# Kernel tuning notes

Measured on AMD Instinct MI355X. Metric: run time of the kernel, lower is better.

The kernel has to match this reference:

```python
import jax, jax.numpy as jnp
import numpy as np

jax.config.update("jax_enable_x64", True)  # int64 needed for packed lattice keys

BILATERAL = True
THETA_ALPHA = 80.0
THETA_BETA = 13.0
THETA_GAMMA = 3.0


def setup_inputs() -> dict:
    key = jax.random.key(0)
    k1, k2 = jax.random.split(key)
    x = jax.random.normal(k1, (2, 21, 256, 256), dtype=jnp.float32)
    image = jax.random.uniform(k2, (2, 3, 256, 256), dtype=jnp.float32) * 255.0  # RGB guide in [0,255)
    return {"x": x, "image": image}


def _permutohedral_filter(vals, feats, bid):
    """Permutohedral lattice Gaussian filtering (Adams et al. / DenseCRF).
    vals: (N, C) float32 signal, feats: (N, d) float32 features, bid: (N,) int64 batch id.
    """
    N, C = vals.shape
    d = feats.shape[1]
    dp1 = d + 1
    # --- elevate features onto the hyperplane sum=0 in R^{d+1} ---
    inv_std = np.sqrt(2.0 / 3.0) * dp1
    scale = (inv_std / np.sqrt((np.arange(d) + 1.0) * (np.arange(d) + 2.0))).astype(np.float32)
    E = np.zeros((dp1, d), np.float32)  # elevation matrix matching DenseCRF recursion
    E[0, :] = 1.0
    for j in range(1, dp1):
        E[j, j:] = 1.0
        E[j, j - 1] = -float(j)
    elevated = (feats * scale) @ E.T  # (N, d+1)

    # --- closest zero-colored lattice point (rem0) and rank ---
    v = elevated / dp1
    up = jnp.ceil(v) * dp1
    down = jnp.floor(v) * dp1
    rem0 = jnp.where(up - elevated < elevated - down, up, down)  # (N, d+1)
    ssum = jnp.round(jnp.sum(rem0, axis=1) / dp1).astype(jnp.int32)  # (N,)

    di = elevated - rem0
    m = jnp.arange(dp1)
    upper = m[None, :] > m[:, None]
    lt = di[:, :, None] < di[:, None, :]
    le = di[:, :, None] <= di[:, None, :]
    contrib = jnp.where(upper[None], lt, le) & (m[None, :] != m[:, None])[None]
    rank = jnp.sum(contrib, axis=2).astype(jnp.int32) + ssum[:, None]  # (N, d+1)
    rem0 = jnp.where(rank < 0, rem0 + dp1, jnp.where(rank > d, rem0 - dp1, rem0))
    rank = jnp.where(rank < 0, rank + dp1, jnp.where(rank > d, rank - dp1, rank))

    # --- barycentric weights (N, d+1) ---
    t = (elevated - rem0) / dp1
    oh = (jax.nn.one_hot(d - rank, d + 2, dtype=vals.dtype)
          - jax.nn.one_hot(d + 1 - rank, d + 2, dtype=vals.dtype))
    bary = jnp.einsum('ni,nij->nj', t, oh)  # (N, d+2)
    bary = jnp.concatenate([bary[:, :1] + 1.0 + bary[:, d + 1:d + 2], bary[:, 1:dp1]], axis=1)

    # --- simplex vertex keys via canonical simplex ---
    rem0i = jnp.round(rem0).astype(jnp.int64)
    r = jnp.arange(dp1, dtype=jnp.int64)
    keys = (rem0i[:, None, :] + r[None, :, None]
            - dp1 * (rank[:, None, :].astype(jnp.int64) > (d - r)[None, :, None]))  # (N, d+1, d+1)

    OFF = jnp.int64(2048)
    BASE = jnp.int64(4096)
    pw = BASE ** jnp.arange(d, dtype=jnp.int64)
    BSHIFT = jnp.int64(4096 ** d)  # batch-id slot above coordinate bits

    def pack(k, b):  # pack first d coords (sum-zero => last is redundant) + batch id
        return jnp.sum((k[..., :d] + OFF) * pw, axis=-1) + b * BSHIFT

    packed = pack(keys, bid[:, None]).reshape(-1)  # (N*(d+1),)
    M = int(packed.shape[0])
    FILL = jnp.iinfo(jnp.int64).max
    uk = jnp.unique(packed, size=M, fill_value=FILL)  # sorted unique lattice keys (hash table)
    idx = jnp.searchsorted(uk, packed)  # (N*(d+1),) index of each vertex

    # --- splat ---
    lat = jnp.zeros((M, C), vals.dtype).at[idx].add(
        (bary[:, :, None] * vals[:, None, :]).reshape(-1, C))

    # decode unique keys back to full (d+1)-dim coords + batch id
    ub = uk // BSHIFT
    remk = uk % BSHIFT
    coords = ((remk[:, None] // pw[None, :]) % BASE) - OFF  # (M, d)
    coords = jnp.concatenate([coords, -jnp.sum(coords, axis=1, keepdims=True)], axis=1)  # (M, d+1)

    def lookup(q, lat_cur):
        pos = jnp.clip(jnp.searchsorted(uk, q), 0, M - 1)
        ok = uk[pos] == q
        return jnp.where(ok[:, None], lat_cur[pos], 0.0)

    # --- blur: [1 2 1]/2 along each of the d+1 lattice directions ---
    for j in range(dp1):
        off = np.ones((dp1,), np.int64)
        off[j] = -d
        off = jnp.asarray(off)
        n1 = pack(coords + off[None, :], ub)
        n2 = pack(coords - off[None, :], ub)
        lat = lat + 0.5 * (lookup(n1, lat) + lookup(n2, lat))

    # --- slice ---
    alpha = 1.0 / (1.0 + 2.0 ** (-d))
    sliced = lat[idx].reshape(N, dp1, C)
    return alpha * jnp.einsum('nr,nrc->nc', bary, sliced)


def _forward(x, image):
    B, C, H, W = x.shape
    x_nhwc = jnp.transpose(x, (0, 2, 3, 1)).reshape(-1, C)
    im_nhwc = jnp.transpose(image, (0, 2, 3, 1))
    ys, xs = jnp.meshgrid(jnp.arange(H, dtype=x.dtype), jnp.arange(W, dtype=x.dtype), indexing='ij')
    if BILATERAL:
        pos = jnp.broadcast_to(jnp.stack([xs, ys], axis=-1) / THETA_ALPHA, (B, H, W, 2))
        feats = jnp.concatenate([pos, im_nhwc / THETA_BETA], axis=-1)  # d = 5
    else:
        feats = jnp.broadcast_to(jnp.stack([xs, ys], axis=-1) / THETA_GAMMA, (B, H, W, 2))  # d = 2
    d = feats.shape[-1]
    bid = jnp.repeat(jnp.arange(B, dtype=jnp.int64), H * W)  # keep per-image lattices separate
    out = _permutohedral_filter(x_nhwc, feats.reshape(B * H * W, d), bid)
    return jnp.transpose(out.reshape(B, H, W, C), (0, 3, 1, 2))


def reference(x, image):
    return _forward(x, image)
```

## Files before the change

kernel.cpp:

```cpp
#include <hip/hip_runtime.h>
#include <hip/hip_fp16.h>
#include <stdint.h>

#define BB   2
#define CC   21
#define HCP  32
#define NPT  (BB*256*256)
#define DP1  6
#define NV   (NPT*DP1)
#define TS   (1u<<20)
#define TMASK (TS-1)
#define EMPTYK 0xFFFFFFFFFFFFFFFFULL
#define NBLK (NV/1024)
#define NBUCK 32768
#define KEYMASK ((1ULL<<41)-1ULL)


__device__ __forceinline__ uint64_t hmix(uint64_t x){
  x ^= x >> 33; x *= 0xff51afd7ed558ccdULL;
  x ^= x >> 33; x *= 0xc4ceb9fe1a85ec53ULL;
  x ^= x >> 33; return x;
}

__device__ __forceinline__ int hlookup(const unsigned long long* __restrict__ hs,
                                       uint64_t key){
  uint32_t h = (uint32_t)hmix(key) & TMASK;
  for (;;){
    unsigned long long e = hs[h];
    if (e == EMPTYK) return -1;
    if ((e & KEYMASK) == (unsigned long long)key) return (int)(e >> 41);
    h = (h + 1) & TMASK;
  }
}

__device__ __forceinline__ void row_load(const __half* p, float2 f[12]){
  const uint4* p4 = (const uint4*)p;
  #pragma unroll
  for (int i=0;i<3;i++){
    uint4 r = p4[i];
    const __half2* h = (const __half2*)&r;
    #pragma unroll
    for (int j=0;j<4;j++) f[i*4+j] = __half22float2(h[j]);
  }
}
__device__ __forceinline__ void row_store(__half* p, const float2 f[12]){
  uint4* p4 = (uint4*)p;
  #pragma unroll
  for (int i=0;i<3;i++){
    uint4 r;
    __half2* h = (__half2*)&r;
    #pragma unroll
    for (int j=0;j<4;j++) h[j] = __floats2half2_rn(f[i*4+j].x, f[i*4+j].y);
    p4[i] = r;
  }
}

__global__ __launch_bounds__(256) void k_tx(const float* __restrict__ xin,
      __half* __restrict__ xt){
  int n = blockIdx.x*256 + threadIdx.x;
  if (n >= NPT) return;
  int b = n >> 16, pix = n & 65535;
  const float* xb = xin + (((size_t)b*CC) << 16) + pix;
  float2 v[12];
  #pragma unroll
  for (int q=0;q<12;q++){
    int c0 = 2*q, c1 = 2*q+1;
    v[q].x = (c0 < CC) ? xb[(size_t)c0 << 16] : 0.f;
    v[q].y = (c1 < CC) ? xb[(size_t)c1 << 16] : 0.f;
  }
  row_store(xt + (size_t)n*HCP, v);
}

__global__ __launch_bounds__(256) void k_build(const float* __restrict__ img,
      unsigned long long* __restrict__ hs,
      int* __restrict__ hist,
      unsigned long long* __restrict__ pkeys,
      float* __restrict__ pbary,
      int* __restrict__ hslot){
  int n = blockIdx.x*256 + threadIdx.x;
  if (n >= NPT) return;
  int b = n >> 16, pix = n & 65535;
  int y = pix >> 8, x = pix & 255;
  const float sc0 = 3.4641016151377544f, sc1 = 2.0f, sc2 = 1.4142135623730951f,
              sc3 = 1.0954451150103321f, sc4 = 0.8944271909999159f;
  size_t ib = ((size_t)b*3) << 16;
  float f0 = ((float)x / 80.0f) * sc0;
  float f1 = ((float)y / 80.0f) * sc1;
  float f2 = (img[ib + pix]          / 13.0f) * sc2;
  float f3 = (img[ib + 65536 + pix]  / 13.0f) * sc3;
  float f4 = (img[ib + 131072 + pix] / 13.0f) * sc4;
  float E[6];
  {
    float s4 = f4;
    E[5] = -5.0f*f4;
    E[4] = -4.0f*f3 + s4;
    float s3 = f3 + s4;
    E[3] = -3.0f*f2 + s3;
    float s2 = f2 + s3;
    E[2] = -2.0f*f1 + s2;
    float s1 = f1 + s2;
    E[1] = -f0 + s1;
    E[0] =  f0 + s1;
  }
  float rem0[6], di[6]; int rk[6];
  float ssf = 0.f;
  #pragma unroll
  for (int i=0;i<6;i++){
    float v  = E[i] / 6.0f;
    float up = ceilf(v)*6.0f, dn = floorf(v)*6.0f;
    float r0 = (up - E[i] < E[i] - dn) ? up : dn;
    rem0[i] = r0; di[i] = E[i] - r0; ssf += r0;
  }
  int ssum = (int)rintf(ssf / 6.0f);
  #pragma unroll
  for (int i=0;i<6;i++){
    int c = ssum;
    #pragma unroll
    for (int k=0;k<6;k++){
      if (k==i) continue;
      bool t = (k>i) ? (di[i] < di[k]) : (di[i] <= di[k]);
      c += t ? 1 : 0;
    }
    rk[i] = c;
  }
  #pragma unroll
  for (int i=0;i<6;i++){
    if      (rk[i] < 0){ rk[i] += 6; rem0[i] += 6.0f; }
    else if (rk[i] > 5){ rk[i] -= 6; rem0[i] -= 6.0f; }
  }
  float bar[7] = {0,0,0,0,0,0,0};
  #pragma unroll
  for (int i=0;i<6;i++){
    float t = (E[i] - rem0[i]) / 6.0f;
    #pragma unroll
    for (int j=0;j<7;j++){
      bar[j] += ((5-rk[i])==j) ? t : 0.0f;
      bar[j] -= ((6-rk[i])==j) ? t : 0.0f;
    }
  }
  float w0 = bar[0] + 1.0f + bar[6];
  int ri[5];
  #pragma unroll
  for (int i=0;i<5;i++) ri[i] = (int)rintf(rem0[i]);
  uint64_t bbit = ((uint64_t)b) << 40;
  #pragma unroll
  for (int r=0;r<6;r++){
    uint64_t key = bbit;
    #pragma unroll
    for (int i=0;i<5;i++){
      int k = ri[i] + r - ((rk[i] > 5-r) ? 6 : 0);
      key |= ((uint64_t)(uint32_t)(k + 128) & 0xFFULL) << (8*i);
    }
    pkeys[n*6+r] = key;
    pbary[n*6+r] = (r==0) ? w0 : bar[r];
    uint64_t ins = key | ((uint64_t)(uint32_t)n << 41);
    uint32_t h = (uint32_t)hmix(key) & TMASK;
    for (;;){
      unsigned long long seen = hs[h];
      if (seen != EMPTYK && (seen & KEYMASK) == (unsigned long long)key) break;
      if (seen == EMPTYK){
        unsigned long long prev = atomicCAS(&hs[h], EMPTYK, (unsigned long long)ins);
        if (prev == EMPTYK){
          atomicAdd(&hist[n >> 2], 1);
          break;
        }
        if ((prev & KEYMASK) == (unsigned long long)key) break;
      }
      h = (h + 1) & TMASK;
    }
    hslot[n*6+r] = (int)h;
  }
}

__global__ __launch_bounds__(1024) void k_scan_small(const int* __restrict__ hist,
      int* __restrict__ boff, int* __restrict__ bcur, int* __restrict__ counter){
  __shared__ int s[1024];
  int t = threadIdx.x;
  int base = t * (NBUCK/1024);
  int loc[NBUCK/1024];
  int sum = 0;
  #pragma unroll
  for (int i=0;i<NBUCK/1024;i++){ loc[i] = hist[base+i]; sum += loc[i]; }
  s[t] = sum;
  __syncthreads();
  #pragma unroll
  for (int o=1;o<1024;o<<=1){
    int add = (t>=o) ? s[t-o] : 0;
    __syncthreads();
    s[t] += add;
    __syncthreads();
  }
  int run = s[t] - sum;
  #pragma unroll
  for (int i=0;i<NBUCK/1024;i++){ boff[base+i] = run; bcur[base+i] = run; run += loc[i]; }
  if (t == 1023) counter[0] = run;
}

__global__ __launch_bounds__(1024) void k_place(unsigned long long* __restrict__ hs,
      int* __restrict__ bcur,
      unsigned long long* __restrict__ latkeys){
  uint32_t s = blockIdx.x*1024 + threadIdx.x;
  unsigned long long e = hs[s];
  if (e == EMPTYK) return;
  int nown = (int)(e >> 41);
  int idx = atomicAdd(&bcur[nown >> 2], 1);
  unsigned long long key = e & KEYMASK;
  hs[s] = key | ((unsigned long long)idx << 41);
  latkeys[idx] = key;
}

__global__ __launch_bounds__(256) void k_nbr(const unsigned long long* __restrict__ hs,
      const unsigned long long* __restrict__ latkeys, const int* __restrict__ counter,
      uint2* __restrict__ nbr){
  int m = blockIdx.x*256 + threadIdx.x;
  if (m >= *counter) return;
  uint64_t key = (uint64_t)latkeys[m];
  const unsigned long long S5 = (1ULL<<32)+(1ULL<<24)+(1ULL<<16)+(1ULL<<8)+1ULL;
  #pragma unroll
  for (int j=0;j<6;j++){
    unsigned long long delta = (j<5) ? (S5 - (6ULL << (8*j))) : S5;
    int i1 = hlookup(hs, key + delta);
    int i2 = hlookup(hs, key - delta);
    nbr[(size_t)j*NV + m] = make_uint2((uint32_t)(i1+1), (uint32_t)(i2+1));
  }
}

__global__ __launch_bounds__(256) void k_find(const unsigned long long* __restrict__ hs,
      const int* __restrict__ hslot,
      int* __restrict__ pidx, int* __restrict__ cnt){
  int t = blockIdx.x*256 + threadIdx.x;
  if (t >= NV) return;
  int i = (int)(hs[hslot[t]] >> 41);
  pidx[t] = i;
  atomicAdd(&cnt[i], 1);
}

__global__ __launch_bounds__(1024) void k_scan1(const int* __restrict__ cnt,
      int* __restrict__ off, int* __restrict__ bsum){
  __shared__ int s[1024];
  int t = threadIdx.x;
  int i = blockIdx.x*1024 + t;
  int v = cnt[i];
  s[t] = v;
  __syncthreads();
  #pragma unroll
  for (int o=1;o<1024;o<<=1){
    int add = (t>=o) ? s[t-o] : 0;
    __syncthreads();
    s[t] += add;
    __syncthreads();
  }
  off[i] = s[t] - v;
  if (t==1023) bsum[blockIdx.x] = s[t];
}

__global__ __launch_bounds__(1024) void k_scan2(int* __restrict__ bsum){
  __shared__ int s[1024];
  int t = threadIdx.x;
  int v = (t < NBLK) ? bsum[t] : 0;
  s[t] = v;
  __syncthreads();
  #pragma unroll
  for (int o=1;o<1024;o<<=1){
    int add = (t>=o) ? s[t-o] : 0;
    __syncthreads();
    s[t] += add;
    __syncthreads();
  }
  if (t < NBLK) bsum[t] = s[t] - v;
}

__global__ __launch_bounds__(1024) void k_scan3(int* __restrict__ off,
      const int* __restrict__ bsum, int* __restrict__ cur){
  int i = blockIdx.x*1024 + threadIdx.x;
  int o = off[i] + bsum[blockIdx.x];
  off[i] = o;
  cur[i] = o;
}

__global__ __launch_bounds__(256) void k_scatter(const int* __restrict__ pidx,
      const float* __restrict__ pbary, int* __restrict__ cur, uint2* __restrict__ plist2){
  int t = blockIdx.x*256 + threadIdx.x;
  if (t >= NV) return;
  int idx = pidx[t];
  int pos = atomicAdd(&cur[idx], 1);
  plist2[pos] = make_uint2((uint32_t)(t/6), __float_as_uint(pbary[t]));
}

__global__ __launch_bounds__(256) void k_splat2(const __half* __restrict__ xt,
      const int* __restrict__ off, const int* __restrict__ cnt,
      const uint2* __restrict__ plist2, const int* __restrict__ counter,
      __half* __restrict__ lat){
  int m = blockIdx.x*256 + threadIdx.x;
  if (m >= *counter) return;
  float2 acc[12];
  #pragma unroll
  for (int q=0;q<12;q++) acc[q] = make_float2(0.f,0.f);
  int c0 = off[m], k = cnt[m];
  for (int e=c0; e<c0+k; ++e){
    uint2 pv = plist2[e];
    float w = __uint_as_float(pv.y);
    float2 xr[12];
    row_load(xt + (size_t)pv.x*HCP, xr);
    #pragma unroll
    for (int q=0;q<12;q++){
      acc[q].x = fmaf(w, xr[q].x, acc[q].x);
      acc[q].y = fmaf(w, xr[q].y, acc[q].y);
    }
  }
  row_store(lat + (size_t)m*HCP, acc);
}

__global__ __launch_bounds__(256) void k_blur(const uint2* __restrict__ nbrj,
      const int* __restrict__ counter, const __half* __restrict__ src,
      __half* __restrict__ dst){
  int m = blockIdx.x*256 + threadIdx.x;
  if (m >= *counter) return;
  uint2 e = nbrj[m];
  float2 a[12], u[12], v[12];
  #pragma unroll
  for (int q=0;q<12;q++){ u[q] = make_float2(0.f,0.f); v[q] = make_float2(0.f,0.f); }
  row_load(src + (size_t)m*HCP, a);
  if (e.x) row_load(src + (size_t)(e.x-1u)*HCP, u);
  if (e.y) row_load(src + (size_t)(e.y-1u)*HCP, v);
  float2 r[12];
  #pragma unroll
  for (int q=0;q<12;q++){
    r[q].x = a[q].x + 0.5f*(u[q].x + v[q].x);
    r[q].y = a[q].y + 0.5f*(u[q].y + v[q].y);
  }
  row_store(dst + (size_t)m*HCP, r);
}

__global__ __launch_bounds__(256) void k_slice(const __half* __restrict__ lat,
      const int* __restrict__ pidx, const float* __restrict__ pbary,
      float* __restrict__ out){
  int n = blockIdx.x*256 + threadIdx.x;
  if (n >= NPT) return;
  float2 acc[12];
  #pragma unroll
  for (int q=0;q<12;q++) acc[q] = make_float2(0.f,0.f);
  #pragma unroll
  for (int r=0;r<6;r++){
    int idx = pidx[n*6+r]; float w = pbary[n*6+r];
    float2 L[12];
    row_load(lat + (size_t)idx*HCP, L);
    #pragma unroll
    for (int q=0;q<12;q++){
      acc[q].x = fmaf(w, L[q].x, acc[q].x);
      acc[q].y = fmaf(w, L[q].y, acc[q].y);
    }
  }
  int b = n >> 16, pix = n & 65535;
  float* ob = out + (((size_t)b*CC) << 16) + pix;
  const float alpha = 0.9696969696969697f;
  #pragma unroll
  for (int c=0;c<CC;c++){
    float val = (c & 1) ? acc[c>>1].y : acc[c>>1].x;
    ob[(size_t)c << 16] = alpha * val;
  }
}

extern "C" void kernel_launch(void* const* d_in, const int* in_sizes, int n_in,
                              void* d_out, int out_size, void* d_ws, size_t ws_size,
                              hipStream_t stream){
  const float* xin = (const float*)d_in[0];
  const float* img = (const float*)d_in[1];
  float* out = (float*)d_out;

  char* p = (char*)d_ws;
  auto carve = [&](size_t bytes)->char*{
    char* r = p; p += (bytes + 255) & ~(size_t)255; return r;
  };
  unsigned long long* hs      = (unsigned long long*)carve((size_t)TS*8);
  unsigned long long* latkeys = (unsigned long long*)carve((size_t)NV*8);
  int*                counter = (int*)               carve(256);
  unsigned long long* pkeys   = (unsigned long long*)carve((size_t)NV*8);
  int*                pidx    = (int*)               carve((size_t)NV*4);
  float*              pbary   = (float*)             carve((size_t)NV*4);
  int*                hslot   = (int*)               carve((size_t)NV*4);
  int*                cnt     = (int*)               carve((size_t)NV*4);
  int*                off     = (int*)               carve((size_t)NV*4);
  int*                cur     = (int*)               carve((size_t)NV*4);
  int*                bsum    = (int*)               carve((size_t)NBLK*4);
  int*                hist    = (int*)               carve((size_t)NBUCK*4);
  int*                boff    = (int*)               carve((size_t)NBUCK*4);
  int*                bcur    = (int*)               carve((size_t)NBUCK*4);
  uint2*              nbr     = (uint2*)             carve((size_t)6*NV*8);
  __half*             latA    = (__half*)            carve((size_t)NV*HCP*2);
  __half*             latB    = (__half*)            carve((size_t)NV*HCP*2);

  __half* xt     = latB;
  uint2* plist2  = (uint2*)pkeys;

  hipMemsetAsync(hs, 0xFF, (size_t)TS*8, stream);
  hipMemsetAsync(cnt, 0, (size_t)NV*4, stream);
  hipMemsetAsync(hist, 0, (size_t)NBUCK*4, stream);

  k_tx        <<<NPT/256, 256, 0, stream>>>(xin, xt);
  k_build     <<<NPT/256, 256, 0, stream>>>(img, hs, hist, pkeys, pbary, hslot);
  k_scan_small<<<1,      1024, 0, stream>>>(hist, boff, bcur, counter);
  k_place     <<<TS/1024,1024, 0, stream>>>(hs, bcur, latkeys);
  k_nbr       <<<NV/256,  256, 0, stream>>>(hs, latkeys, counter, nbr);
  k_find      <<<NV/256,  256, 0, stream>>>(hs, hslot, pidx, cnt);
  k_scan1     <<<NBLK,   1024, 0, stream>>>(cnt, off, bsum);
  k_scan2     <<<1,      1024, 0, stream>>>(bsum);
  k_scan3     <<<NBLK,   1024, 0, stream>>>(off, bsum, cur);
  k_scatter   <<<NV/256,  256, 0, stream>>>(pidx, pbary, cur, plist2);
  k_splat2    <<<NV/256,  256, 0, stream>>>(xt, off, cnt, plist2, counter, latA);

  __half* src = latA; __half* dst = latB;
  for (int j=0;j<6;j++){
    k_blur<<<NV/256, 256, 0, stream>>>(nbr + (size_t)j*NV, counter, src, dst);
    __half* tmp = src; src = dst; dst = tmp;
  }
  k_slice<<<NPT/256, 256, 0, stream>>>(src, pidx, pbary, out);
}
```

Baseline: 373.5 us.

## Halve neighbor lookups via reverse-edge scatter and use block-local histogram in build

The neighbor kernel now performs only the +delta hash lookup for each lattice vertex and records the reverse (-delta) neighbor by scattering into a second array, which halves hash probes. This replaces the interleaved uint2 neighbor array with two separate arrays that must be zero-initialized. The build kernel drops the unused per-point key output, goes straight to atomicCAS without a preceding plain read, and accumulates its bucket histogram in shared memory before writing it out once per block. The extra memset and the scattered writes add some traffic, and the CAS-first probing loop may cause more atomic contention on keys that are already present.

After: 376.1 us. Within noise of the previous version (+0.7%).

```diff
diff --git a/kernel.cpp b/kernel.cpp
--- a/kernel.cpp
+++ b/kernel.cpp
@@ -74,11 +74,13 @@
 __global__ __launch_bounds__(256) void k_build(const float* __restrict__ img,
       unsigned long long* __restrict__ hs,
       int* __restrict__ hist,
-      unsigned long long* __restrict__ pkeys,
       float* __restrict__ pbary,
       int* __restrict__ hslot){
-  int n = blockIdx.x*256 + threadIdx.x;
-  if (n >= NPT) return;
+  __shared__ int s_hist[64];
+  int t = threadIdx.x;
+  if (t < 64) s_hist[t] = 0;
+  __syncthreads();
+  int n = blockIdx.x*256 + t;
   int b = n >> 16, pix = n & 65535;
   int y = pix >> 8, x = pix & 255;
   const float sc0 = 3.4641016151377544f, sc1 = 2.0f, sc2 = 1.4142135623730951f,
@@ -118,8 +120,8 @@
     #pragma unroll
     for (int k=0;k<6;k++){
       if (k==i) continue;
-      bool t = (k>i) ? (di[i] < di[k]) : (di[i] <= di[k]);
-      c += t ? 1 : 0;
+      bool tt = (k>i) ? (di[i] < di[k]) : (di[i] <= di[k]);
+      c += tt ? 1 : 0;
     }
     rk[i] = c;
   }
@@ -131,11 +133,11 @@
   float bar[7] = {0,0,0,0,0,0,0};
   #pragma unroll
   for (int i=0;i<6;i++){
-    float t = (E[i] - rem0[i]) / 6.0f;
+    float tb = (E[i] - rem0[i]) / 6.0f;
     #pragma unroll
     for (int j=0;j<7;j++){
-      bar[j] += ((5-rk[i])==j) ? t : 0.0f;
-      bar[j] -= ((6-rk[i])==j) ? t : 0.0f;
+      bar[j] += ((5-rk[i])==j) ? tb : 0.0f;
+      bar[j] -= ((6-rk[i])==j) ? tb : 0.0f;
     }
   }
   float w0 = bar[0] + 1.0f + bar[6];
@@ -151,25 +153,22 @@
       int k = ri[i] + r - ((rk[i] > 5-r) ? 6 : 0);
       key |= ((uint64_t)(uint32_t)(k + 128) & 0xFFULL) << (8*i);
     }
-    pkeys[n*6+r] = key;
     pbary[n*6+r] = (r==0) ? w0 : bar[r];
     uint64_t ins = key | ((uint64_t)(uint32_t)n << 41);
     uint32_t h = (uint32_t)hmix(key) & TMASK;
     for (;;){
-      unsigned long long seen = hs[h];
-      if (seen != EMPTYK && (seen & KEYMASK) == (unsigned long long)key) break;
-      if (seen == EMPTYK){
-        unsigned long long prev = atomicCAS(&hs[h], EMPTYK, (unsigned long long)ins);
-        if (prev == EMPTYK){
-          atomicAdd(&hist[n >> 2], 1);
-          break;
-        }
-        if ((prev & KEYMASK) == (unsigned long long)key) break;
+      unsigned long long prev = atomicCAS(&hs[h], EMPTYK, (unsigned long long)ins);
+      if (prev == EMPTYK){
+        atomicAdd(&s_hist[t >> 2], 1);
+        break;
       }
+      if ((prev & KEYMASK) == (unsigned long long)key) break;
       h = (h + 1) & TMASK;
     }
     hslot[n*6+r] = (int)h;
   }
+  __syncthreads();
+  if (t < 64) hist[blockIdx.x*64 + t] = s_hist[t];
 }
 
 __global__ __launch_bounds__(1024) void k_scan_small(const int* __restrict__ hist,
@@ -211,7 +210,7 @@
 
 __global__ __launch_bounds__(256) void k_nbr(const unsigned long long* __restrict__ hs,
       const unsigned long long* __restrict__ latkeys, const int* __restrict__ counter,
-      uint2* __restrict__ nbr){
+      uint32_t* __restrict__ nbrx, uint32_t* __restrict__ nbry){
   int m = blockIdx.x*256 + threadIdx.x;
   if (m >= *counter) return;
   uint64_t key = (uint64_t)latkeys[m];
@@ -220,8 +219,8 @@
   for (int j=0;j<6;j++){
     unsigned long long delta = (j<5) ? (S5 - (6ULL << (8*j))) : S5;
     int i1 = hlookup(hs, key + delta);
-    int i2 = hlookup(hs, key - delta);
-    nbr[(size_t)j*NV + m] = make_uint2((uint32_t)(i1+1), (uint32_t)(i2+1));
+    nbrx[(size_t)j*NV + m] = (uint32_t)(i1+1);
+    if (i1 >= 0) nbry[(size_t)j*NV + (uint32_t)i1] = (uint32_t)(m+1);
   }
 }
 
@@ -311,18 +310,19 @@
   row_store(lat + (size_t)m*HCP, acc);
 }
 
-__global__ __launch_bounds__(256) void k_blur(const uint2* __restrict__ nbrj,
+__global__ __launch_bounds__(256) void k_blur(const uint32_t* __restrict__ nx,
+      const uint32_t* __restrict__ ny,
       const int* __restrict__ counter, const __half* __restrict__ src,
       __half* __restrict__ dst){
   int m = blockIdx.x*256 + threadIdx.x;
   if (m >= *counter) return;
-  uint2 e = nbrj[m];
+  uint32_t ex = nx[m], ey = ny[m];
   float2 a[12], u[12], v[12];
   #pragma unroll
   for (int q=0;q<12;q++){ u[q] = make_float2(0.f,0.f); v[q] = make_float2(0.f,0.f); }
   row_load(src + (size_t)m*HCP, a);
-  if (e.x) row_load(src + (size_t)(e.x-1u)*HCP, u);
-  if (e.y) row_load(src + (size_t)(e.y-1u)*HCP, v);
+  if (ex) row_load(src + (size_t)(ex-1u)*HCP, u);
+  if (ey) row_load(src + (size_t)(ey-1u)*HCP, v);
   float2 r[12];
   #pragma unroll
   for (int q=0;q<12;q++){
@@ -375,7 +375,7 @@
   unsigned long long* hs      = (unsigned long long*)carve((size_t)TS*8);
   unsigned long long* latkeys = (unsigned long long*)carve((size_t)NV*8);
   int*                counter = (int*)               carve(256);
-  unsigned long long* pkeys   = (unsigned long long*)carve((size_t)NV*8);
+  uint2*              plist2  = (uint2*)             carve((size_t)NV*8);
   int*                pidx    = (int*)               carve((size_t)NV*4);
   float*              pbary   = (float*)             carve((size_t)NV*4);
   int*                hslot   = (int*)               carve((size_t)NV*4);
@@ -386,22 +386,22 @@
   int*                hist    = (int*)               carve((size_t)NBUCK*4);
   int*                boff    = (int*)               carve((size_t)NBUCK*4);
   int*                bcur    = (int*)               carve((size_t)NBUCK*4);
-  uint2*              nbr     = (uint2*)             carve((size_t)6*NV*8);
+  uint32_t*           nbrx    = (uint32_t*)          carve((size_t)6*NV*4);
+  uint32_t*           nbry    = (uint32_t*)          carve((size_t)6*NV*4);
   __half*             latA    = (__half*)            carve((size_t)NV*HCP*2);
   __half*             latB    = (__half*)            carve((size_t)NV*HCP*2);
 
-  __half* xt     = latB;
-  uint2* plist2  = (uint2*)pkeys;
+  __half* xt = latB;
 
   hipMemsetAsync(hs, 0xFF, (size_t)TS*8, stream);
   hipMemsetAsync(cnt, 0, (size_t)NV*4, stream);
-  hipMemsetAsync(hist, 0, (size_t)NBUCK*4, stream);
+  hipMemsetAsync(nbry, 0, (size_t)6*NV*4, stream);
 
   k_tx        <<<NPT/256, 256, 0, stream>>>(xin, xt);
-  k_build     <<<NPT/256, 256, 0, stream>>>(img, hs, hist, pkeys, pbary, hslot);
+  k_build     <<<NPT/256, 256, 0, stream>>>(img, hs, hist, pbary, hslot);
   k_scan_small<<<1,      1024, 0, stream>>>(hist, boff, bcur, counter);
   k_place     <<<TS/1024,1024, 0, stream>>>(hs, bcur, latkeys);
-  k_nbr       <<<NV/256,  256, 0, stream>>>(hs, latkeys, counter, nbr);
+  k_nbr       <<<NV/256,  256, 0, stream>>>(hs, latkeys, counter, nbrx, nbry);
   k_find      <<<NV/256,  256, 0, stream>>>(hs, hslot, pidx, cnt);
   k_scan1     <<<NBLK,   1024, 0, stream>>>(cnt, off, bsum);
   k_scan2     <<<1,      1024, 0, stream>>>(bsum);
@@ -411,7 +411,8 @@
 
   __half* src = latA; __half* dst = latB;
   for (int j=0;j<6;j++){
-    k_blur<<<NV/256, 256, 0, stream>>>(nbr + (size_t)j*NV, counter, src, dst);
+    k_blur<<<NV/256, 256, 0, stream>>>(nbrx + (size_t)j*NV, nbry + (size_t)j*NV,
+                                       counter, src, dst);
     __half* tmp = src; src = dst; dst = tmp;
   }
   k_slice<<<NPT/256, 256, 0, stream>>>(src, pidx, pbary, out);
```
